# Performance work log

Hardware: AMD Instinct MI355X
Metric: run time of the kernel (lower is better)

## Reference

```python
import jax, jax.numpy as jnp
import numpy as np

D_MODEL = 768
N_HEADS = 12
D_K = D_MODEL // N_HEADS


def setup_inputs() -> dict:
    key = jax.random.key(0)
    ks = jax.random.split(key, 11)
    B, T = 4, 2048
    s = 1.0 / np.sqrt(D_K)
    so = 1.0 / np.sqrt(D_MODEL)
    return {
        "q": jax.random.normal(ks[0], (B, T, D_MODEL), jnp.float32),
        "k": jax.random.normal(ks[1], (B, T, D_MODEL), jnp.float32),
        "v": jax.random.normal(ks[2], (B, T, D_MODEL), jnp.float32),
        "Wq": jax.random.normal(ks[3], (D_K, D_K), jnp.float32) * s,
        "bq": jax.random.normal(ks[4], (D_K,), jnp.float32) * s,
        "Wk": jax.random.normal(ks[5], (D_K, D_K), jnp.float32) * s,
        "bk": jax.random.normal(ks[6], (D_K,), jnp.float32) * s,
        "Wv": jax.random.normal(ks[7], (D_K, D_K), jnp.float32) * s,
        "bv": jax.random.normal(ks[8], (D_K,), jnp.float32) * s,
        "Wo": jax.random.normal(ks[9], (D_MODEL, D_MODEL), jnp.float32) * so,
        "bo": jax.random.normal(ks[10], (D_MODEL,), jnp.float32) * so,
    }


def reference(q, k, v, Wq, bq, Wk, bk, Wv, bv, Wo, bo):
    B, T, _ = q.shape
    # split into heads: [B, T, H, d_k]; per-head Linear shares weights across heads
    qh = q.reshape(B, T, N_HEADS, D_K)
    kh = k.reshape(B, T, N_HEADS, D_K)
    vh = v.reshape(B, T, N_HEADS, D_K)
    # torch Linear: x @ W^T + b, then transpose to [B, H, T, d_k]
    qh = jnp.einsum("bthd,ed->bhte", qh, Wq) + bq
    kh = jnp.einsum("bthd,ed->bhte", kh, Wk) + bk
    vh = jnp.einsum("bthd,ed->bhte", vh, Wv) + bv
    # scaled dot-product attention, full [B,H,T,T] scores (faithful to source)
    scores = jnp.einsum("bhqd,bhkd->bhqk", qh, kh) / jnp.sqrt(
        jnp.asarray(D_K, qh.dtype)
    )
    attn = jax.nn.softmax(scores, axis=-1)
    # einsum 'ijkl,ijlr->ikjr' -> output laid out [B, T, H, d_k]
    out_h = jnp.einsum("bhqk,bhkd->bqhd", attn, vh)
    concat = out_h.reshape(B, T, D_MODEL)
    return concat @ Wo.T + bo
```

## Files before the change

kernel.cpp:

```cpp
#include <hip/hip_runtime.h>


#define T_SEQ  2048
#define NH     12
#define DK     64
#define DMODEL 768
#define BATCH  4

typedef __attribute__((ext_vector_type(8))) short short8;
typedef __attribute__((ext_vector_type(4))) float f32x4;
typedef __attribute__((ext_vector_type(4))) unsigned short us4;

__device__ __forceinline__ float bf2f(unsigned short u) {
  union { unsigned int i; float f; } x; x.i = ((unsigned int)u) << 16; return x.f;
}
__device__ __forceinline__ unsigned short f2bf(float f) {
  union { float f; unsigned int i; } x; x.f = f;
  unsigned int r = x.i + 0x7fffu + ((x.i >> 16) & 1u);
  return (unsigned short)(r >> 16);
}
__device__ __forceinline__ us4 f4_to_bf4(float4 v) {
  us4 r; r.x = f2bf(v.x); r.y = f2bf(v.y); r.z = f2bf(v.z); r.w = f2bf(v.w); return r;
}


__global__ __launch_bounds__(256, 4)
void qkv_proj_kernel(const float* __restrict__ qin,
                     const float* __restrict__ kin,
                     const float* __restrict__ vin,
                     const float* __restrict__ Wq, const float* __restrict__ bq,
                     const float* __restrict__ Wk, const float* __restrict__ bk,
                     const float* __restrict__ Wv, const float* __restrict__ bv,
                     unsigned short* __restrict__ Qp,
                     unsigned short* __restrict__ Kp,
                     unsigned short* __restrict__ Vt)
{
  const int tt  = blockIdx.x;
  const int bh  = blockIdx.y;
  const int p   = blockIdx.z;
  const int b   = bh / NH, h = bh % NH;
  const int t0  = tt * 64;
  const int tid = threadIdx.x;
  const int wv  = tid >> 6;
  const int ln  = tid & 63;
  const int c   = ln & 15;
  const int qd  = ln >> 4;

  __shared__ __align__(16) unsigned short sX[64 * 72];
  __shared__ __align__(16) unsigned short sW[64 * 72];
  __shared__ __align__(16) unsigned short sVtr[64 * 68];

  const float* in = (p == 0) ? qin : (p == 1) ? kin : vin;
  const float* W  = (p == 0) ? Wq  : (p == 1) ? Wk  : Wv;
  const float* bs = (p == 0) ? bq  : (p == 1) ? bk  : bv;

  const int r0 = tid >> 4, g = tid & 15;
#pragma unroll
  for (int l = 0; l < 4; ++l) {
    int r = l * 16 + r0;
    float4 xv = *reinterpret_cast<const float4*>(in + ((size_t)(b * T_SEQ + t0 + r)) * DMODEL + h * DK + g * 4);
    *reinterpret_cast<us4*>(&sX[r * 72 + g * 4]) = f4_to_bf4(xv);
    float4 wvv = *reinterpret_cast<const float4*>(W + r * DK + g * 4);
    *reinterpret_cast<us4*>(&sW[r * 72 + g * 4]) = f4_to_bf4(wvv);
  }
  __syncthreads();

  short8 af[2];
#pragma unroll
  for (int kc = 0; kc < 2; ++kc)
    af[kc] = *reinterpret_cast<const short8*>(&sX[(wv * 16 + c) * 72 + kc * 32 + qd * 8]);

  f32x4 acc[4];
#pragma unroll
  for (int nb = 0; nb < 4; ++nb) {
    f32x4 a = {0.f, 0.f, 0.f, 0.f};
#pragma unroll
    for (int kc = 0; kc < 2; ++kc) {
      short8 bf = *reinterpret_cast<const short8*>(&sW[(nb * 16 + c) * 72 + kc * 32 + qd * 8]);
      a = __builtin_amdgcn_mfma_f32_16x16x32_bf16(af[kc], bf, a, 0, 0, 0);
    }
    acc[nb] = a;
  }

  if (p < 2) {
    unsigned short* outp = (p == 0) ? Qp : Kp;
#pragma unroll
    for (int nb = 0; nb < 4; ++nb) {
      int n = nb * 16 + c;
      float bias = bs[n];
#pragma unroll
      for (int r = 0; r < 4; ++r) {
        int t = t0 + wv * 16 + qd * 4 + r;
        outp[((size_t)bh * T_SEQ + t) * DK + n] = f2bf(acc[nb][r] + bias);
      }
    }
  } else {
#pragma unroll
    for (int nb = 0; nb < 4; ++nb) {
      int n = nb * 16 + c;
      float bias = bs[n];
#pragma unroll
      for (int r = 0; r < 4; ++r) {
        int row = wv * 16 + qd * 4 + r;
        sVtr[n * 68 + row] = f2bf(acc[nb][r] + bias);
      }
    }
    __syncthreads();
#pragma unroll
    for (int l = 0; l < 4; ++l) {
      int d = l * 16 + r0;
      us4 val = *reinterpret_cast<const us4*>(&sVtr[d * 68 + g * 4]);
      *reinterpret_cast<us4*>(Vt + ((size_t)bh * DK + d) * T_SEQ + t0 + g * 4) = val;
    }
  }
}

__global__ __launch_bounds__(256, 3)
void flash_kernel(const unsigned short* __restrict__ Qp,
                  const unsigned short* __restrict__ Kp,
                  const unsigned short* __restrict__ Vt,
                  unsigned short* __restrict__ concat)
{
  const int qt  = blockIdx.x;
  const int bh  = blockIdx.y;
  const int b   = bh / NH, h = bh % NH;
  const int tid = threadIdx.x;
  const int wv  = tid >> 6;
  const int ln  = tid & 63;
  const int c   = ln & 15;
  const int qd  = ln >> 4;

  __shared__ __align__(16) unsigned short sK[64 * 72];
  __shared__ __align__(16) unsigned short sV[64 * 72];
  __shared__ __align__(16) unsigned short sP[4][2][16 * 72];

  const int row0 = qt * 128 + wv * 32;

  short8 qf[2][2];
#pragma unroll
  for (int f = 0; f < 2; ++f) {
    const unsigned short* qb = Qp + ((size_t)bh * T_SEQ + row0 + f * 16 + c) * DK + qd * 8;
    qf[f][0] = *reinterpret_cast<const short8*>(qb);
    qf[f][1] = *reinterpret_cast<const short8*>(qb + 32);
  }

  const int r0 = tid >> 4, g = tid & 15;
  us4 kreg[4], vreg[4];
#define LOAD_TILE(J)                                                                   \
  {                                                                                    \
    _Pragma("unroll")                                                                  \
    for (int l = 0; l < 4; ++l) {                                                      \
      int r = l * 16 + r0;                                                             \
      kreg[l] = *reinterpret_cast<const us4*>(Kp + ((size_t)bh * T_SEQ + (J) * 64 + r) * DK + g * 4); \
      vreg[l] = *reinterpret_cast<const us4*>(Vt + ((size_t)bh * DK + r) * T_SEQ + (J) * 64 + g * 4); \
    }                                                                                  \
  }

  LOAD_TILE(0);

  f32x4 o[2][4];
  float lsum[2] = {0.f, 0.f};
#pragma unroll
  for (int f = 0; f < 2; ++f)
#pragma unroll
    for (int nb = 0; nb < 4; ++nb) o[f][nb] = (f32x4){0.f, 0.f, 0.f, 0.f};

  const float cexp = 0.125f * 1.44269504088896340736f;

  for (int j = 0; j < T_SEQ / 64; ++j) {
    __syncthreads();
#pragma unroll
    for (int l = 0; l < 4; ++l) {
      int r = l * 16 + r0;
      *reinterpret_cast<us4*>(&sK[r * 72 + g * 4]) = kreg[l];
      *reinterpret_cast<us4*>(&sV[r * 72 + g * 4]) = vreg[l];
    }
    __syncthreads();

    int jn = (j + 1) & (T_SEQ / 64 - 1);
    LOAD_TILE(jn);

    short8 kf[4][2];
#pragma unroll
    for (int nb = 0; nb < 4; ++nb) {
      kf[nb][0] = *reinterpret_cast<const short8*>(&sK[(nb * 16 + c) * 72 + qd * 8]);
      kf[nb][1] = *reinterpret_cast<const short8*>(&sK[(nb * 16 + c) * 72 + 32 + qd * 8]);
    }

    f32x4 st[2][4];
#pragma unroll
    for (int f = 0; f < 2; ++f)
#pragma unroll
      for (int nb = 0; nb < 4; ++nb) {
        f32x4 a = {0.f, 0.f, 0.f, 0.f};
        a = __builtin_amdgcn_mfma_f32_16x16x32_bf16(kf[nb][0], qf[f][0], a, 0, 0, 0);
        a = __builtin_amdgcn_mfma_f32_16x16x32_bf16(kf[nb][1], qf[f][1], a, 0, 0, 0);
        st[f][nb] = a;
      }

#pragma unroll
    for (int f = 0; f < 2; ++f) {
#pragma unroll
      for (int nb = 0; nb < 4; ++nb) {
        float p0 = __builtin_amdgcn_exp2f(st[f][nb][0] * cexp);
        float p1 = __builtin_amdgcn_exp2f(st[f][nb][1] * cexp);
        float p2 = __builtin_amdgcn_exp2f(st[f][nb][2] * cexp);
        float p3 = __builtin_amdgcn_exp2f(st[f][nb][3] * cexp);
        lsum[f] += (p0 + p1) + (p2 + p3);
        us4 pk; pk.x = f2bf(p0); pk.y = f2bf(p1); pk.z = f2bf(p2); pk.w = f2bf(p3);
        *reinterpret_cast<us4*>(&sP[wv][f][c * 72 + nb * 16 + qd * 4]) = pk;
      }
    }

    short8 pf[2][2];
#pragma unroll
    for (int f = 0; f < 2; ++f) {
      pf[f][0] = *reinterpret_cast<const short8*>(&sP[wv][f][c * 72 + qd * 8]);
      pf[f][1] = *reinterpret_cast<const short8*>(&sP[wv][f][c * 72 + 32 + qd * 8]);
    }

    short8 vf[4][2];
#pragma unroll
    for (int nb = 0; nb < 4; ++nb) {
      vf[nb][0] = *reinterpret_cast<const short8*>(&sV[(nb * 16 + c) * 72 + qd * 8]);
      vf[nb][1] = *reinterpret_cast<const short8*>(&sV[(nb * 16 + c) * 72 + 32 + qd * 8]);
    }

#pragma unroll
    for (int f = 0; f < 2; ++f)
#pragma unroll
      for (int nb = 0; nb < 4; ++nb) {
        o[f][nb] = __builtin_amdgcn_mfma_f32_16x16x32_bf16(pf[f][0], vf[nb][0], o[f][nb], 0, 0, 0);
        o[f][nb] = __builtin_amdgcn_mfma_f32_16x16x32_bf16(pf[f][1], vf[nb][1], o[f][nb], 0, 0, 0);
      }
  }

#pragma unroll
  for (int f = 0; f < 2; ++f) {
    lsum[f] += __shfl_xor(lsum[f], 16, 64);
    lsum[f] += __shfl_xor(lsum[f], 32, 64);
  }

#pragma unroll
  for (int f = 0; f < 2; ++f) {
#pragma unroll
    for (int r = 0; r < 4; ++r) {
      float lr = __shfl(lsum[f], qd * 4 + r, 16);
      int t = row0 + f * 16 + qd * 4 + r;
#pragma unroll
      for (int nb = 0; nb < 4; ++nb) {
        float val = o[f][nb][r] / lr;
        concat[((size_t)(b * T_SEQ + t)) * DMODEL + h * DK + nb * 16 + c] = f2bf(val);
      }
    }
  }
#undef LOAD_TILE
}

__global__ __launch_bounds__(256, 3)
void oproj_kernel(const unsigned short* __restrict__ A,
                  const float* __restrict__ Wo,
                  const float* __restrict__ bo,
                  float* __restrict__ out)
{
  const int nt  = blockIdx.x;
  const int mt  = blockIdx.y;
  const int tid = threadIdx.x;
  const int wv  = tid >> 6;
  const int ln  = tid & 63;
  const int c   = ln & 15;
  const int qd  = ln >> 4;

  __shared__ __align__(16) unsigned short sA[128 * 72];
  __shared__ __align__(16) unsigned short sB[64 * 72];

  const int r0 = tid >> 4, g = tid & 15;
  us4 areg[8];
  float4 breg[4];
#define LOAD_K(KK)                                                                       \
  {                                                                                      \
    _Pragma("unroll")                                                                    \
    for (int l = 0; l < 8; ++l)                                                          \
      areg[l] = *reinterpret_cast<const us4*>(A + ((size_t)(mt * 128 + l * 16 + r0)) * DMODEL + (KK) * 64 + g * 4); \
    _Pragma("unroll")                                                                    \
    for (int l = 0; l < 4; ++l)                                                          \
      breg[l] = *reinterpret_cast<const float4*>(Wo + ((size_t)(nt * 64 + l * 16 + r0)) * DMODEL + (KK) * 64 + g * 4); \
  }

  LOAD_K(0);

  f32x4 acc[2][4];
#pragma unroll
  for (int f = 0; f < 2; ++f)
#pragma unroll
    for (int nb = 0; nb < 4; ++nb) acc[f][nb] = (f32x4){0.f, 0.f, 0.f, 0.f};

  for (int kk = 0; kk < DMODEL / 64; ++kk) {
    __syncthreads();
#pragma unroll
    for (int l = 0; l < 8; ++l)
      *reinterpret_cast<us4*>(&sA[(l * 16 + r0) * 72 + g * 4]) = areg[l];
#pragma unroll
    for (int l = 0; l < 4; ++l)
      *reinterpret_cast<us4*>(&sB[(l * 16 + r0) * 72 + g * 4]) = f4_to_bf4(breg[l]);
    __syncthreads();

    int kn = kk + 1 < DMODEL / 64 ? kk + 1 : 0;
    LOAD_K(kn);

    short8 af[2][2];
#pragma unroll
    for (int f = 0; f < 2; ++f) {
      af[f][0] = *reinterpret_cast<const short8*>(&sA[(wv * 32 + f * 16 + c) * 72 + qd * 8]);
      af[f][1] = *reinterpret_cast<const short8*>(&sA[(wv * 32 + f * 16 + c) * 72 + 32 + qd * 8]);
    }
#pragma unroll
    for (int nb = 0; nb < 4; ++nb) {
      short8 b0 = *reinterpret_cast<const short8*>(&sB[(nb * 16 + c) * 72 + qd * 8]);
      short8 b1 = *reinterpret_cast<const short8*>(&sB[(nb * 16 + c) * 72 + 32 + qd * 8]);
#pragma unroll
      for (int f = 0; f < 2; ++f) {
        acc[f][nb] = __builtin_amdgcn_mfma_f32_16x16x32_bf16(af[f][0], b0, acc[f][nb], 0, 0, 0);
        acc[f][nb] = __builtin_amdgcn_mfma_f32_16x16x32_bf16(af[f][1], b1, acc[f][nb], 0, 0, 0);
      }
    }
  }

#pragma unroll
  for (int f = 0; f < 2; ++f)
#pragma unroll
    for (int nb = 0; nb < 4; ++nb) {
      int n = nt * 64 + nb * 16 + c;
      float bias = bo[n];
#pragma unroll
      for (int r = 0; r < 4; ++r) {
        int m = mt * 128 + wv * 32 + f * 16 + qd * 4 + r;
        out[(size_t)m * DMODEL + n] = acc[f][nb][r] + bias;
      }
    }
#undef LOAD_K
}

extern "C" void kernel_launch(void* const* d_in, const int* in_sizes, int n_in,
                              void* d_out, int out_size, void* d_ws, size_t ws_size,
                              hipStream_t stream) {
  const float* q  = (const float*)d_in[0];
  const float* k  = (const float*)d_in[1];
  const float* v  = (const float*)d_in[2];
  const float* Wq = (const float*)d_in[3];
  const float* bq = (const float*)d_in[4];
  const float* Wk = (const float*)d_in[5];
  const float* bk = (const float*)d_in[6];
  const float* Wv = (const float*)d_in[7];
  const float* bv = (const float*)d_in[8];
  const float* Wo = (const float*)d_in[9];
  const float* bo = (const float*)d_in[10];

  const size_t NTOK = (size_t)BATCH * T_SEQ;
  const size_t PER  = NTOK * DK * NH;
  unsigned short* Qp     = (unsigned short*)d_ws;
  unsigned short* Kp     = Qp + PER;
  unsigned short* Vt     = Kp + PER;
  unsigned short* concat = Vt + PER;

  dim3 blk(256);
  qkv_proj_kernel<<<dim3(32, BATCH * NH, 3), blk, 0, stream>>>(q, k, v, Wq, bq, Wk, bk, Wv, bv, Qp, Kp, Vt);
  flash_kernel<<<dim3(16, BATCH * NH), blk, 0, stream>>>(Qp, Kp, Vt, concat);
  oproj_kernel<<<dim3(12, 64), blk, 0, stream>>>(concat, Wo, bo, (float*)d_out);
}
```

Measured before the change: 234.9 us.

## Keep softmax probabilities in registers via permlane swaps and double-buffer K/V tiles

The flash kernel now rearranges the exp'd scores into MFMA A-operand layout with permlane32/16 swaps, so it no longer round-trips them through LDS. The row sums are computed by an MFMA against a ones vector, which removes the scalar accumulation and the final shuffles. K/V shared tiles are double-buffered so each iteration needs only one barrier. Other changes: the softmax scale is folded into the Q projection, bf16 conversion uses the hardware v_cvt_pk_bf16_f32 instruction, and blocks are remapped so that the heads sharing K/V are grouped per XCD. The trade-offs are extra LDS for the second buffer, bf16-rounded row sums, and reliance on gfx950-specific permlane intrinsics.

Result: faster. 213.9 us (-8.9%).

```diff
diff --git a/kernel.cpp b/kernel.cpp
--- a/kernel.cpp
+++ b/kernel.cpp
@@ -11,16 +11,23 @@
 typedef __attribute__((ext_vector_type(4))) float f32x4;
 typedef __attribute__((ext_vector_type(4))) unsigned short us4;
 
-__device__ __forceinline__ float bf2f(unsigned short u) {
-  union { unsigned int i; float f; } x; x.i = ((unsigned int)u) << 16; return x.f;
-}
-__device__ __forceinline__ unsigned short f2bf(float f) {
-  union { float f; unsigned int i; } x; x.f = f;
-  unsigned int r = x.i + 0x7fffu + ((x.i >> 16) & 1u);
-  return (unsigned short)(r >> 16);
+#define CEXP (0.125f * 1.44269504088896340736f)
+
+__device__ __forceinline__ unsigned cvt_pk_bf16(float lo, float hi) {
+  unsigned r;
+  asm("v_cvt_pk_bf16_f32 %0, %1, %2" : "=v"(r) : "v"(lo), "v"(hi));
+  return r;
+}
+__device__ __forceinline__ unsigned short f2bf1(float f) {
+  unsigned r;
+  asm("v_cvt_pk_bf16_f32 %0, %1, %1" : "=v"(r) : "v"(f));
+  return (unsigned short)r;
 }
 __device__ __forceinline__ us4 f4_to_bf4(float4 v) {
-  us4 r; r.x = f2bf(v.x); r.y = f2bf(v.y); r.z = f2bf(v.z); r.w = f2bf(v.w); return r;
+  union { unsigned u[2]; us4 r; } t;
+  t.u[0] = cvt_pk_bf16(v.x, v.y);
+  t.u[1] = cvt_pk_bf16(v.z, v.w);
+  return t.r;
 }
 
 
@@ -84,25 +91,26 @@
 
   if (p < 2) {
     unsigned short* outp = (p == 0) ? Qp : Kp;
+    const float sc = (p == 0) ? CEXP : 1.0f;
+#pragma unroll
+    for (int nb = 0; nb < 4; ++nb) {
+      int n = nb * 16 + c;
+      float bias = bs[n] * sc;
+#pragma unroll
+      for (int r = 0; r < 4; ++r) {
+        int t = t0 + wv * 16 + qd * 4 + r;
+        outp[((size_t)bh * T_SEQ + t) * DK + n] = f2bf1(fmaf(acc[nb][r], sc, bias));
+      }
+    }
+  } else {
 #pragma unroll
     for (int nb = 0; nb < 4; ++nb) {
       int n = nb * 16 + c;
       float bias = bs[n];
 #pragma unroll
       for (int r = 0; r < 4; ++r) {
-        int t = t0 + wv * 16 + qd * 4 + r;
-        outp[((size_t)bh * T_SEQ + t) * DK + n] = f2bf(acc[nb][r] + bias);
-      }
-    }
-  } else {
-#pragma unroll
-    for (int nb = 0; nb < 4; ++nb) {
-      int n = nb * 16 + c;
-      float bias = bs[n];
-#pragma unroll
-      for (int r = 0; r < 4; ++r) {
         int row = wv * 16 + qd * 4 + r;
-        sVtr[n * 68 + row] = f2bf(acc[nb][r] + bias);
+        sVtr[n * 68 + row] = f2bf1(acc[nb][r] + bias);
       }
     }
     __syncthreads();
@@ -121,8 +129,11 @@
                   const unsigned short* __restrict__ Vt,
                   unsigned short* __restrict__ concat)
 {
-  const int qt  = blockIdx.x;
-  const int bh  = blockIdx.y;
+  const int lin = blockIdx.y * 16 + blockIdx.x;
+  const int xcd = lin & 7;
+  const int li  = lin >> 3;
+  const int bh  = xcd * 6 + (li >> 4);
+  const int qt  = li & 15;
   const int b   = bh / NH, h = bh % NH;
   const int tid = threadIdx.x;
   const int wv  = tid >> 6;
@@ -130,9 +141,8 @@
   const int c   = ln & 15;
   const int qd  = ln >> 4;
 
-  __shared__ __align__(16) unsigned short sK[64 * 72];
-  __shared__ __align__(16) unsigned short sV[64 * 72];
-  __shared__ __align__(16) unsigned short sP[4][2][16 * 72];
+  __shared__ __align__(16) unsigned short sK[2][64 * 72];
+  __shared__ __align__(16) unsigned short sV[2][64 * 72];
 
   const int row0 = qt * 128 + wv * 32;
 
@@ -149,81 +159,100 @@
 #define LOAD_TILE(J)                                                                   \
   {                                                                                    \
     _Pragma("unroll")                                                                  \
-    for (int l = 0; l < 4; ++l) {                                                      \
-      int r = l * 16 + r0;                                                             \
-      kreg[l] = *reinterpret_cast<const us4*>(Kp + ((size_t)bh * T_SEQ + (J) * 64 + r) * DK + g * 4); \
-      vreg[l] = *reinterpret_cast<const us4*>(Vt + ((size_t)bh * DK + r) * T_SEQ + (J) * 64 + g * 4); \
+    for (int l_ = 0; l_ < 4; ++l_) {                                                   \
+      int r_ = l_ * 16 + r0;                                                           \
+      kreg[l_] = *reinterpret_cast<const us4*>(Kp + ((size_t)bh * T_SEQ + (J) * 64 + r_) * DK + g * 4); \
+      vreg[l_] = *reinterpret_cast<const us4*>(Vt + ((size_t)bh * DK + r_) * T_SEQ + (J) * 64 + g * 4); \
     }                                                                                  \
   }
+#define WRITE_BUF(B)                                                                   \
+  {                                                                                    \
+    _Pragma("unroll")                                                                  \
+    for (int l_ = 0; l_ < 4; ++l_) {                                                   \
+      int r_ = l_ * 16 + r0;                                                           \
+      *reinterpret_cast<us4*>(&sK[B][r_ * 72 + g * 4]) = kreg[l_];                     \
+      *reinterpret_cast<us4*>(&sV[B][r_ * 72 + g * 4]) = vreg[l_];                     \
+    }                                                                                  \
+  }
 
   LOAD_TILE(0);
+  WRITE_BUF(0);
+  LOAD_TILE(1);
 
   f32x4 o[2][4];
-  float lsum[2] = {0.f, 0.f};
-#pragma unroll
-  for (int f = 0; f < 2; ++f)
+  f32x4 lacc[2];
+#pragma unroll
+  for (int f = 0; f < 2; ++f) {
+    lacc[f] = (f32x4){0.f, 0.f, 0.f, 0.f};
 #pragma unroll
     for (int nb = 0; nb < 4; ++nb) o[f][nb] = (f32x4){0.f, 0.f, 0.f, 0.f};
-
-  const float cexp = 0.125f * 1.44269504088896340736f;
+  }
+
+  short8 ones;
+#pragma unroll
+  for (int i = 0; i < 8; ++i) ones[i] = (short)0x3F80;
 
   for (int j = 0; j < T_SEQ / 64; ++j) {
     __syncthreads();
-#pragma unroll
-    for (int l = 0; l < 4; ++l) {
-      int r = l * 16 + r0;
-      *reinterpret_cast<us4*>(&sK[r * 72 + g * 4]) = kreg[l];
-      *reinterpret_cast<us4*>(&sV[r * 72 + g * 4]) = vreg[l];
-    }
-    __syncthreads();
-
-    int jn = (j + 1) & (T_SEQ / 64 - 1);
-    LOAD_TILE(jn);
+    const int cur = j & 1;
+    WRITE_BUF((j + 1) & 1);
+    LOAD_TILE((j + 2) & (T_SEQ / 64 - 1));
 
     short8 kf[4][2];
 #pragma unroll
     for (int nb = 0; nb < 4; ++nb) {
-      kf[nb][0] = *reinterpret_cast<const short8*>(&sK[(nb * 16 + c) * 72 + qd * 8]);
-      kf[nb][1] = *reinterpret_cast<const short8*>(&sK[(nb * 16 + c) * 72 + 32 + qd * 8]);
-    }
-
-    f32x4 st[2][4];
-#pragma unroll
-    for (int f = 0; f < 2; ++f)
+      kf[nb][0] = *reinterpret_cast<const short8*>(&sK[cur][(nb * 16 + c) * 72 + qd * 8]);
+      kf[nb][1] = *reinterpret_cast<const short8*>(&sK[cur][(nb * 16 + c) * 72 + 32 + qd * 8]);
+    }
+
+    short8 pf[2][2];
+#pragma unroll
+    for (int f = 0; f < 2; ++f) {
+      f32x4 stf[4];
 #pragma unroll
       for (int nb = 0; nb < 4; ++nb) {
         f32x4 a = {0.f, 0.f, 0.f, 0.f};
         a = __builtin_amdgcn_mfma_f32_16x16x32_bf16(kf[nb][0], qf[f][0], a, 0, 0, 0);
         a = __builtin_amdgcn_mfma_f32_16x16x32_bf16(kf[nb][1], qf[f][1], a, 0, 0, 0);
-        st[f][nb] = a;
-      }
+        stf[nb] = a;
+      }
+      unsigned pk[4][2];
+#pragma unroll
+      for (int nb = 0; nb < 4; ++nb) {
+        float p0 = __builtin_amdgcn_exp2f(stf[nb][0]);
+        float p1 = __builtin_amdgcn_exp2f(stf[nb][1]);
+        float p2 = __builtin_amdgcn_exp2f(stf[nb][2]);
+        float p3 = __builtin_amdgcn_exp2f(stf[nb][3]);
+        pk[nb][0] = cvt_pk_bf16(p0, p1);
+        pk[nb][1] = cvt_pk_bf16(p2, p3);
+      }
+#pragma unroll
+      for (int kc = 0; kc < 2; ++kc) {
+        union { unsigned w[4]; short8 s; } u;
+#pragma unroll
+        for (int pr = 0; pr < 2; ++pr) {
+          unsigned X = pk[2 * kc][pr];
+          unsigned Y = pk[2 * kc + 1][pr];
+          auto s32 = __builtin_amdgcn_permlane32_swap(X, Y, false, false);
+          auto s16 = __builtin_amdgcn_permlane16_swap(s32[0], s32[1], false, false);
+          u.w[pr]     = s16[0];
+          u.w[2 + pr] = s16[1];
+        }
+        pf[f][kc] = u.s;
+      }
+    }
+
+    short8 vf[4][2];
+#pragma unroll
+    for (int nb = 0; nb < 4; ++nb) {
+      vf[nb][0] = *reinterpret_cast<const short8*>(&sV[cur][(nb * 16 + c) * 72 + qd * 8]);
+      vf[nb][1] = *reinterpret_cast<const short8*>(&sV[cur][(nb * 16 + c) * 72 + 32 + qd * 8]);
+    }
 
 #pragma unroll
     for (int f = 0; f < 2; ++f) {
-#pragma unroll
-      for (int nb = 0; nb < 4; ++nb) {
-        float p0 = __builtin_amdgcn_exp2f(st[f][nb][0] * cexp);
-        float p1 = __builtin_amdgcn_exp2f(st[f][nb][1] * cexp);
-        float p2 = __builtin_amdgcn_exp2f(st[f][nb][2] * cexp);
-        float p3 = __builtin_amdgcn_exp2f(st[f][nb][3] * cexp);
-        lsum[f] += (p0 + p1) + (p2 + p3);
-        us4 pk; pk.x = f2bf(p0); pk.y = f2bf(p1); pk.z = f2bf(p2); pk.w = f2bf(p3);
-        *reinterpret_cast<us4*>(&sP[wv][f][c * 72 + nb * 16 + qd * 4]) = pk;
-      }
-    }
-
-    short8 pf[2][2];
-#pragma unroll
-    for (int f = 0; f < 2; ++f) {
-      pf[f][0] = *reinterpret_cast<const short8*>(&sP[wv][f][c * 72 + qd * 8]);
-      pf[f][1] = *reinterpret_cast<const short8*>(&sP[wv][f][c * 72 + 32 + qd * 8]);
-    }
-
-    short8 vf[4][2];
-#pragma unroll
-    for (int nb = 0; nb < 4; ++nb) {
-      vf[nb][0] = *reinterpret_cast<const short8*>(&sV[(nb * 16 + c) * 72 + qd * 8]);
-      vf[nb][1] = *reinterpret_cast<const short8*>(&sV[(nb * 16 + c) * 72 + 32 + qd * 8]);
+      lacc[f] = __builtin_amdgcn_mfma_f32_16x16x32_bf16(pf[f][0], ones, lacc[f], 0, 0, 0);
+      lacc[f] = __builtin_amdgcn_mfma_f32_16x16x32_bf16(pf[f][1], ones, lacc[f], 0, 0, 0);
     }
 
 #pragma unroll
@@ -237,24 +266,21 @@
 
 #pragma unroll
   for (int f = 0; f < 2; ++f) {
-    lsum[f] += __shfl_xor(lsum[f], 16, 64);
-    lsum[f] += __shfl_xor(lsum[f], 32, 64);
-  }
-
-#pragma unroll
-  for (int f = 0; f < 2; ++f) {
+    float linv[4];
+#pragma unroll
+    for (int r = 0; r < 4; ++r) linv[r] = __builtin_amdgcn_rcpf(lacc[f][r]);
 #pragma unroll
     for (int r = 0; r < 4; ++r) {
-      float lr = __shfl(lsum[f], qd * 4 + r, 16);
       int t = row0 + f * 16 + qd * 4 + r;
 #pragma unroll
       for (int nb = 0; nb < 4; ++nb) {
-        float val = o[f][nb][r] / lr;
-        concat[((size_t)(b * T_SEQ + t)) * DMODEL + h * DK + nb * 16 + c] = f2bf(val);
+        concat[((size_t)(b * T_SEQ + t)) * DMODEL + h * DK + nb * 16 + c] =
+            f2bf1(o[f][nb][r] * linv[r]);
       }
     }
   }
 #undef LOAD_TILE
+#undef WRITE_BUF
 }
 
 __global__ __launch_bounds__(256, 3)
```
